# Optimization experiments

Hardware: AMD Instinct MI355X
Metric: run time of the kernel (lower is better)

Reference implementation:

```python
import jax, jax.numpy as jnp
import numpy as np

H, W = 200, 200          # detector resolution
DELX, DELY = 2.0, 2.0    # detector pixel size
EPS = 1e-8


def _rotation(theta, phi, gamma):
    # R = Rz(theta) @ Ry(phi) @ Rx(gamma), as in diffdrr's Rxyz
    ct, st = jnp.cos(theta), jnp.sin(theta)
    cp, sp = jnp.cos(phi), jnp.sin(phi)
    cg, sg = jnp.cos(gamma), jnp.sin(gamma)
    one, zero = jnp.ones_like(ct), jnp.zeros_like(ct)
    Rz = jnp.stack([jnp.stack([ct, -st, zero]), jnp.stack([st, ct, zero]), jnp.stack([zero, zero, one])])
    Ry = jnp.stack([jnp.stack([cp, zero, sp]), jnp.stack([zero, one, zero]), jnp.stack([-sp, zero, cp])])
    Rx = jnp.stack([jnp.stack([one, zero, zero]), jnp.stack([zero, cg, -sg]), jnp.stack([zero, sg, cg])])
    return Rz @ Ry @ Rx


def setup_inputs() -> dict:
    key = jax.random.key(0)
    volume = jax.random.uniform(key, (256, 256, 256), dtype=jnp.float32)
    spacing = jnp.ones((3,), dtype=jnp.float32)
    return {
        "volume": volume,
        "spacing": spacing,
        "sdr": jnp.float32(300.0),
        "theta": jnp.float32(np.pi),
        "phi": jnp.float32(0.0),
        "gamma": jnp.float32(np.pi / 2),
        "bx": jnp.float32(128.0),
        "by": jnp.float32(128.0),
        "bz": jnp.float32(128.0),
    }


def _drr_forward(volume, spacing, sdr, theta, phi, gamma, bx, by, bz):
    # DRR.__init__ flips the volume along axis 0
    vol = volume[::-1]
    nxyz = np.array(vol.shape)  # static shapes: (X, Y, Z)

    # ---- Detector.make_xrays: camera basis, source and detector plane ----
    R = sdr * _rotation(theta, phi, gamma)          # (3,3)
    source = R[:, 0]                                # rho * first column
    center = -source
    u, v = R[:, 1] / sdr, R[:, 2] / sdr             # unit in-plane basis
    t = (jnp.arange(-(H // 2), H // 2) + 1).astype(jnp.float32) * DELX
    s = (jnp.arange(-(W // 2), W // 2) + 1).astype(jnp.float32) * DELY
    trans = jnp.stack([bx, by, bz])
    src = source + trans                            # (3,)
    # cartesian_prod(t, s): row-major (t slow, s fast) -> (H*W, 3)
    tgt = (t[:, None, None] * u + s[None, :, None] * v + center + trans).reshape(H * W, 3)

    # ---- Siddon.raytrace ----
    sdd = tgt - src + EPS                           # (n, 3)
    # alpha values at every axis-aligned voxel boundary plane
    ax = (jnp.arange(nxyz[0] + 1, dtype=jnp.float32) * spacing[0] - src[0]) / sdd[:, 0:1]
    ay = (jnp.arange(nxyz[1] + 1, dtype=jnp.float32) * spacing[1] - src[1]) / sdd[:, 1:2]
    az = (jnp.arange(nxyz[2] + 1, dtype=jnp.float32) * spacing[2] - src[2]) / sdd[:, 2:3]
    alphas = jnp.concatenate([ax, ay, az], axis=-1)  # (n, P) with P = X+Y+Z+3

    # entry/exit alphas of the volume bounding box
    a0 = (0.0 - src) / sdd                           # (n, 3)
    a1 = (nxyz.astype(np.float32) * spacing - src) / sdd
    amin = jnp.max(jnp.minimum(a0, a1), axis=-1, keepdims=True)
    amax = jnp.min(jnp.maximum(a0, a1), axis=-1, keepdims=True)

    good = (alphas >= amin) & (alphas <= amax)
    alphas = jnp.sort(jnp.where(good, alphas, jnp.inf), axis=-1)  # invalid -> +inf at end

    amid = 0.5 * (alphas[:, :-1] + alphas[:, 1:])    # (n, P-1)
    step = alphas[:, 1:] - alphas[:, :-1]            # inf-inf -> nan for padding
    valid = jnp.isfinite(step)

    # midpoint positions -> voxel indices (trunc, as in torch .trunc())
    pts = src + amid[..., None] * sdd[:, None, :]    # (n, P-1, 3)
    idx = jnp.trunc(jnp.where(valid[..., None], pts, 0.0) / spacing).astype(jnp.int32)
    idx = jnp.clip(idx, 0, jnp.asarray(nxyz - 1, dtype=jnp.int32))
    vox = vol[idx[..., 0], idx[..., 1], idx[..., 2]]  # (n, P-1) gather

    drr = jnp.sum(jnp.where(valid, step, 0.0) * vox, axis=-1)  # nansum equivalent
    drr = drr * jnp.linalg.norm(tgt - src + EPS, axis=-1)       # scale by ray length
    return drr.reshape(1, 1, H, W)


def reference(volume, spacing, sdr, theta, phi, gamma, bx, by, bz):
    return _drr_forward(volume, spacing, sdr, theta, phi, gamma, bx, by, bz)
```

## Files before the change

### kernel.cpp

```cpp
#include <hip/hip_runtime.h>
#include <math.h>

#pragma clang fp contract(off)

#define SPLIT 13
#define BATCH 8
static constexpr int HH = 200, WW = 200;
static constexpr int NRAY = HH * WW;
static constexpr int RBLK = 157;
static constexpr int NWG  = RBLK * SPLIT;

__device__ __forceinline__ float alpha_of(float k, float sp, float src, float sdd) {
    return (k * sp - src) / sdd;
}

__device__ __forceinline__ int seed_ptr(float X, float spv, float sr, float sd, bool pos) {
    const float kf = (X * sd + sr) / spv;
    int kk;
    if (pos) {
        kk = (int)floorf(kf) + 1;
        kk = kk < 0 ? 0 : (kk > 257 ? 257 : kk);
        while (kk > 0    && alpha_of((float)(kk-1), spv, sr, sd) >  X) --kk;
        while (kk <= 256 && alpha_of((float)kk,     spv, sr, sd) <= X) ++kk;
    } else {
        kk = (int)ceilf(kf) - 1;
        kk = kk > 256 ? 256 : (kk < -1 ? -1 : kk);
        while (kk < 256 && alpha_of((float)(kk+1), spv, sr, sd) >  X) ++kk;
        while (kk >= 0  && alpha_of((float)kk,     spv, sr, sd) <= X) --kk;
    }
    return kk;
}

#define GEN_INTERVAL(stepv, offv)                                        \
    {   const float q = fminf(fminf(tM0, tM1), tM2);                     \
        stepv = q - prev;                                                \
        const float amid = 0.5f * (prev + q);                            \
        const float p0 = src0 + amid * sdd0;                             \
        const float p1 = src1 + amid * sdd1;                             \
        const float p2 = src2 + amid * sdd2;                             \
        float f0, f1, f2;                                                \
        if (UNIT) { f0 = p0; f1 = p1; f2 = p2; }                         \
        else      { f0 = p0 / spn0; f1 = p1 / spn1; f2 = p2 / spn2; }    \
        f0 = fminf(fmaxf(f0, 0.0f), 255.0f);                             \
        f1 = fminf(fmaxf(f1, 0.0f), 255.0f);                             \
        f2 = fminf(fmaxf(f2, 0.0f), 255.0f);                             \
        const int i0 = (int)f0, i1 = (int)f1, i2 = (int)f2;              \
        offv = (unsigned)(((((255 ^ i0) << 8) + i1) << 8) + i2) << 2;    \
        prev = q;                                                        \
        const bool m0 = (tM0 == q);                                      \
        const bool m1 = !m0 && (tM1 == q);                               \
        const bool m2 = !(m0 || m1);                                     \
        tM0 = m0 ? tM0 + dl0 : tM0;                                      \
        tM1 = m1 ? tM1 + dl1 : tM1;                                      \
        tM2 = m2 ? tM2 + dl2 : tM2; }

template<bool UNIT>
__device__ __forceinline__ float merge_loop(
    const float* __restrict__ vol, int trip, float prev,
    float tM0, float tM1, float tM2,
    float dl0, float dl1, float dl2,
    float src0, float src1, float src2,
    float spn0, float spn1, float spn2,
    float sdd0, float sdd1, float sdd2)
{
    float acc = 0.0f;
    int n = trip;
    while (n >= BATCH) {
        float stepv[BATCH], vox[BATCH];
        unsigned off[BATCH];
        #pragma unroll
        for (int i = 0; i < BATCH; ++i) {
            GEN_INTERVAL(stepv[i], off[i])
            asm volatile("global_load_dword %0, %1, %2"
                         : "=v"(vox[i])
                         : "v"(off[i]), "s"(vol));
        }
        asm volatile("s_waitcnt vmcnt(0)");
        __builtin_amdgcn_sched_barrier(0);
        #pragma unroll
        for (int i = 0; i < BATCH; ++i)
            acc = fmaf(stepv[i], vox[i], acc);
        n -= BATCH;
    }
    while (n > 0) {
        float stepv;
        unsigned off;
        GEN_INTERVAL(stepv, off)
        const float vox = vol[off >> 2];
        acc = fmaf(stepv, vox, acc);
        --n;
    }
    return acc;
}

__global__ __launch_bounds__(256)
void drr_kernel(const float* __restrict__ vol,
                const float* __restrict__ spacing,
                const float* __restrict__ sdrP,
                const float* __restrict__ thetaP,
                const float* __restrict__ phiP,
                const float* __restrict__ gammaP,
                const float* __restrict__ bxP,
                const float* __restrict__ byP,
                const float* __restrict__ bzP,
                float* __restrict__ out)
{
    const int lin = blockIdx.x;
    const int xcd = lin & 7;
    const int pos = lin >> 3;
    const int swz = (xcd == 0) ? pos : (256 + (xcd - 1) * 255 + pos);
    const int ridBlk = swz / SPLIT;
    const int seg    = swz - ridBlk * SPLIT;

    const int rid = ridBlk * 256 + threadIdx.x;
    if (rid >= NRAY) return;
    const int it  = rid % HH;
    const int is  = rid / HH;

    const float sdr = sdrP[0];
    const float th = thetaP[0], ph = phiP[0], ga = gammaP[0];
    const float ct = cosf(th), st = sinf(th);
    const float cp = cosf(ph), sp = sinf(ph);
    const float cg = cosf(ga), sg = sinf(ga);

    const float rot[3][3] = {
        { ct*cp, ct*sp*sg - st*cg, ct*sp*cg + st*sg },
        { st*cp, st*sp*sg + ct*cg, st*sp*cg - ct*sg },
        { -sp,   cp*sg,            cp*cg            }
    };

    float u[3], v[3], source[3], trans[3], src[3], spn[3];
    trans[0] = bxP[0]; trans[1] = byP[0]; trans[2] = bzP[0];
    for (int a = 0; a < 3; ++a) {
        source[a] = sdr * rot[a][0];
        u[a] = (sdr * rot[a][1]) / sdr;
        v[a] = (sdr * rot[a][2]) / sdr;
        src[a] = source[a] + trans[a];
        spn[a] = spacing[a];
    }

    const float tc = (float)(it - HH/2 + 1) * 2.0f;
    const float sc = (float)(is - WW/2 + 1) * 2.0f;

    float sdd[3];
    float nrm2 = 0.0f;
    for (int a = 0; a < 3; ++a) {
        float tg = tc * u[a] + sc * v[a];
        tg = tg - source[a];
        tg = tg + trans[a];
        float dd = (tg - src[a]) + 1e-8f;
        sdd[a] = dd;
        nrm2 = nrm2 + dd * dd;
    }
    const bool unit = (spn[0] == 1.0f) & (spn[1] == 1.0f) & (spn[2] == 1.0f);

    float amin = -INFINITY, amax = INFINITY;
    for (int a = 0; a < 3; ++a) {
        float a0 = (0.0f - src[a]) / sdd[a];
        float a1 = (256.0f * spn[a] - src[a]) / sdd[a];
        amin = fmaxf(amin, fminf(a0, a1));
        amax = fminf(amax, fmaxf(a0, a1));
    }

    float acc = 0.0f;
    if (amax > amin) {
        const float blo = (seg == 0) ? amin
                        : amin + (amax - amin) * ((float)seg / (float)SPLIT);
        const float bhi = (seg == SPLIT - 1) ? amax
                        : amin + (amax - amin) * ((float)(seg + 1) / (float)SPLIT);

        float tM[3], dl[3];
        float prev = -INFINITY;
        int trip = 0;

        for (int a = 0; a < 3; ++a) {
            const float sd = sdd[a], sr = src[a], spv = spn[a];
            const bool pos2 = sd > 0.0f;
            const int ks = seed_ptr(blo, spv, sr, sd, pos2);
            const int ke = seed_ptr(bhi, spv, sr, sd, pos2);
            int cnt;
            if (pos2) {
                cnt = ke - ks;
                if (ks - 1 >= 0) {
                    const float ap = alpha_of((float)(ks-1), spv, sr, sd);
                    if (ap >= amin && ap > prev) prev = ap;
                }
                tM[a] = (ks <= 256) ? alpha_of((float)ks, spv, sr, sd) : INFINITY;
            } else {
                cnt = ks - ke;
                if (ks + 1 <= 256) {
                    const float ap = alpha_of((float)(ks+1), spv, sr, sd);
                    if (ap >= amin && ap > prev) prev = ap;
                }
                tM[a] = (ks >= 0) ? alpha_of((float)ks, spv, sr, sd) : INFINITY;
            }
            if (cnt < 0) cnt = 0;
            trip += cnt;
            dl[a] = fabsf(spv / sd);
        }

        if (unit) {
            acc = merge_loop<true >(vol, trip, prev,
                                    tM[0], tM[1], tM[2], dl[0], dl[1], dl[2],
                                    src[0], src[1], src[2],
                                    spn[0], spn[1], spn[2],
                                    sdd[0], sdd[1], sdd[2]);
        } else {
            acc = merge_loop<false>(vol, trip, prev,
                                    tM[0], tM[1], tM[2], dl[0], dl[1], dl[2],
                                    src[0], src[1], src[2],
                                    spn[0], spn[1], spn[2],
                                    sdd[0], sdd[1], sdd[2]);
        }
    }

    atomicAdd(&out[it * WW + is], acc * sqrtf(nrm2));
}

extern "C" void kernel_launch(void* const* d_in, const int* in_sizes, int n_in,
                              void* d_out, int out_size, void* d_ws, size_t ws_size,
                              hipStream_t stream)
{
    const float* vol     = (const float*)d_in[0];
    const float* spacing = (const float*)d_in[1];
    const float* sdr     = (const float*)d_in[2];
    const float* theta   = (const float*)d_in[3];
    const float* phi     = (const float*)d_in[4];
    const float* gamma   = (const float*)d_in[5];
    const float* bx      = (const float*)d_in[6];
    const float* by      = (const float*)d_in[7];
    const float* bz      = (const float*)d_in[8];
    float* out = (float*)d_out;

    hipMemsetAsync(out, 0, (size_t)out_size * sizeof(float), stream);

    drr_kernel<<<NWG, 256, 0, stream>>>(vol, spacing, sdr, theta, phi, gamma,
                                        bx, by, bz, out);
}
```

Before: 55.15 us.

## Split DRR into precompute, main trace, and deterministic reduction kernels

```diff
diff --git a/kernel.cpp b/kernel.cpp
--- a/kernel.cpp
+++ b/kernel.cpp
@@ -9,6 +9,16 @@
 static constexpr int NRAY = HH * WW;
 static constexpr int RBLK = 157;
 static constexpr int NWG  = RBLK * SPLIT;
+
+static constexpr int WS_SDD0 = 0;
+static constexpr int WS_SDD1 = NRAY;
+static constexpr int WS_SDD2 = 2 * NRAY;
+static constexpr int WS_AMIN = 3 * NRAY;
+static constexpr int WS_AMAX = 4 * NRAY;
+static constexpr int WS_NORM = 5 * NRAY;
+static constexpr int WS_UNI  = 6 * NRAY;
+static constexpr int WS_PART = 6 * NRAY + 8;
+static constexpr size_t WS_BYTES = (size_t)(WS_PART + SPLIT * NRAY) * 4;
 
 __device__ __forceinline__ float alpha_of(float k, float sp, float src, float sdd) {
     return (k * sp - src) / sdd;
@@ -94,16 +104,75 @@
 }
 
 __global__ __launch_bounds__(256)
-void drr_kernel(const float* __restrict__ vol,
-                const float* __restrict__ spacing,
-                const float* __restrict__ sdrP,
-                const float* __restrict__ thetaP,
-                const float* __restrict__ phiP,
-                const float* __restrict__ gammaP,
-                const float* __restrict__ bxP,
-                const float* __restrict__ byP,
-                const float* __restrict__ bzP,
-                float* __restrict__ out)
+void drr_pre(const float* __restrict__ spacing,
+             const float* __restrict__ sdrP,  const float* __restrict__ thetaP,
+             const float* __restrict__ phiP,  const float* __restrict__ gammaP,
+             const float* __restrict__ bxP,   const float* __restrict__ byP,
+             const float* __restrict__ bzP,   float* __restrict__ ws)
+{
+    const int rid = blockIdx.x * blockDim.x + threadIdx.x;
+    if (rid >= NRAY) return;
+    const int it = rid % HH, is = rid / HH;
+
+    const float sdr = sdrP[0];
+    const float th = thetaP[0], ph = phiP[0], ga = gammaP[0];
+    const float ct = cosf(th), st = sinf(th);
+    const float cp = cosf(ph), sp = sinf(ph);
+    const float cg = cosf(ga), sg = sinf(ga);
+
+    const float rot[3][3] = {
+        { ct*cp, ct*sp*sg - st*cg, ct*sp*cg + st*sg },
+        { st*cp, st*sp*sg + ct*cg, st*sp*cg - ct*sg },
+        { -sp,   cp*sg,            cp*cg            }
+    };
+
+    float u[3], v[3], source[3], trans[3], src[3], spn[3];
+    trans[0] = bxP[0]; trans[1] = byP[0]; trans[2] = bzP[0];
+    for (int a = 0; a < 3; ++a) {
+        source[a] = sdr * rot[a][0];
+        u[a] = (sdr * rot[a][1]) / sdr;
+        v[a] = (sdr * rot[a][2]) / sdr;
+        src[a] = source[a] + trans[a];
+        spn[a] = spacing[a];
+    }
+
+    const float tc = (float)(it - HH/2 + 1) * 2.0f;
+    const float sc = (float)(is - WW/2 + 1) * 2.0f;
+
+    float sdd[3];
+    float nrm2 = 0.0f;
+    for (int a = 0; a < 3; ++a) {
+        float tg = tc * u[a] + sc * v[a];
+        tg = tg - source[a];
+        tg = tg + trans[a];
+        float dd = (tg - src[a]) + 1e-8f;
+        sdd[a] = dd;
+        nrm2 = nrm2 + dd * dd;
+    }
+
+    float amin = -INFINITY, amax = INFINITY;
+    for (int a = 0; a < 3; ++a) {
+        float a0 = (0.0f - src[a]) / sdd[a];
+        float a1 = (256.0f * spn[a] - src[a]) / sdd[a];
+        amin = fmaxf(amin, fminf(a0, a1));
+        amax = fminf(amax, fmaxf(a0, a1));
+    }
+
+    ws[WS_SDD0 + rid] = sdd[0];
+    ws[WS_SDD1 + rid] = sdd[1];
+    ws[WS_SDD2 + rid] = sdd[2];
+    ws[WS_AMIN + rid] = amin;
+    ws[WS_AMAX + rid] = amax;
+    ws[WS_NORM + rid] = sqrtf(nrm2);
+    if (rid == 0) {
+        ws[WS_UNI + 0] = src[0]; ws[WS_UNI + 1] = src[1]; ws[WS_UNI + 2] = src[2];
+        ws[WS_UNI + 3] = spn[0]; ws[WS_UNI + 4] = spn[1]; ws[WS_UNI + 5] = spn[2];
+    }
+}
+
+__global__ __launch_bounds__(256)
+void drr_main(const float* __restrict__ vol,
+              float* __restrict__ ws)
 {
     const int lin = blockIdx.x;
     const int xcd = lin & 7;
@@ -114,21 +183,111 @@
 
     const int rid = ridBlk * 256 + threadIdx.x;
     if (rid >= NRAY) return;
-    const int it  = rid % HH;
-    const int is  = rid / HH;
+
+    const float sdd0 = ws[WS_SDD0 + rid];
+    const float sdd1 = ws[WS_SDD1 + rid];
+    const float sdd2 = ws[WS_SDD2 + rid];
+    const float amin = ws[WS_AMIN + rid];
+    const float amax = ws[WS_AMAX + rid];
+    const float src0 = ws[WS_UNI + 0], src1 = ws[WS_UNI + 1], src2 = ws[WS_UNI + 2];
+    const float spn0 = ws[WS_UNI + 3], spn1 = ws[WS_UNI + 4], spn2 = ws[WS_UNI + 5];
+    const bool unit = (spn0 == 1.0f) & (spn1 == 1.0f) & (spn2 == 1.0f);
+
+    float acc = 0.0f;
+    if (amax > amin) {
+        const float blo = (seg == 0) ? amin
+                        : amin + (amax - amin) * ((float)seg / (float)SPLIT);
+        const float bhi = (seg == SPLIT - 1) ? amax
+                        : amin + (amax - amin) * ((float)(seg + 1) / (float)SPLIT);
+
+        const float sddv[3] = { sdd0, sdd1, sdd2 };
+        const float srcv[3] = { src0, src1, src2 };
+        const float spnv[3] = { spn0, spn1, spn2 };
+        float tM[3], dl[3];
+        float prev = -INFINITY;
+        int trip = 0;
+
+        for (int a = 0; a < 3; ++a) {
+            const float sd = sddv[a], sr = srcv[a], spv = spnv[a];
+            const bool pos2 = sd > 0.0f;
+            const int ks = seed_ptr(blo, spv, sr, sd, pos2);
+            const int ke = seed_ptr(bhi, spv, sr, sd, pos2);
+            int cnt;
+            if (pos2) {
+                cnt = ke - ks;
+                if (ks - 1 >= 0) {
+                    const float ap = alpha_of((float)(ks-1), spv, sr, sd);
+                    if (ap >= amin && ap > prev) prev = ap;
+                }
+                tM[a] = (ks <= 256) ? alpha_of((float)ks, spv, sr, sd) : INFINITY;
+            } else {
+                cnt = ks - ke;
+                if (ks + 1 <= 256) {
+                    const float ap = alpha_of((float)(ks+1), spv, sr, sd);
+                    if (ap >= amin && ap > prev) prev = ap;
+                }
+                tM[a] = (ks >= 0) ? alpha_of((float)ks, spv, sr, sd) : INFINITY;
+            }
+            if (cnt < 0) cnt = 0;
+            trip += cnt;
+            dl[a] = fabsf(spv / sd);
+        }
+
+        if (unit) {
+            acc = merge_loop<true >(vol, trip, prev, tM[0], tM[1], tM[2],
+                                    dl[0], dl[1], dl[2], src0, src1, src2,
+                                    spn0, spn1, spn2, sdd0, sdd1, sdd2);
+        } else {
+            acc = merge_loop<false>(vol, trip, prev, tM[0], tM[1], tM[2],
+                                    dl[0], dl[1], dl[2], src0, src1, src2,
+                                    spn0, spn1, spn2, sdd0, sdd1, sdd2);
+        }
+    }
+
+    ws[WS_PART + seg * NRAY + rid] = acc;
+}
+
+__global__ __launch_bounds__(256)
+void drr_fin(const float* __restrict__ ws, float* __restrict__ out)
+{
+    const int rid = blockIdx.x * blockDim.x + threadIdx.x;
+    if (rid >= NRAY) return;
+    float s = 0.0f;
+    #pragma unroll
+    for (int seg = 0; seg < SPLIT; ++seg)
+        s = s + ws[WS_PART + seg * NRAY + rid];
+    const int it = rid % HH, is = rid / HH;
+    out[it * WW + is] = s * ws[WS_NORM + rid];
+}
+
+__global__ __launch_bounds__(256)
+void drr_mono(const float* __restrict__ vol,
+              const float* __restrict__ spacing,
+              const float* __restrict__ sdrP,  const float* __restrict__ thetaP,
+              const float* __restrict__ phiP,  const float* __restrict__ gammaP,
+              const float* __restrict__ bxP,   const float* __restrict__ byP,
+              const float* __restrict__ bzP,   float* __restrict__ out)
+{
+    const int lin = blockIdx.x;
+    const int xcd = lin & 7;
+    const int pos = lin >> 3;
+    const int swz = (xcd == 0) ? pos : (256 + (xcd - 1) * 255 + pos);
+    const int ridBlk = swz / SPLIT;
+    const int seg    = swz - ridBlk * SPLIT;
+    const int rid = ridBlk * 256 + threadIdx.x;
+    if (rid >= NRAY) return;
+    const int it = rid % HH, is = rid / HH;
 
     const float sdr = sdrP[0];
     const float th = thetaP[0], ph = phiP[0], ga = gammaP[0];
     const float ct = cosf(th), st = sinf(th);
     const float cp = cosf(ph), sp = sinf(ph);
     const float cg = cosf(ga), sg = sinf(ga);
-
     const float rot[3][3] = {
         { ct*cp, ct*sp*sg - st*cg, ct*sp*cg + st*sg },
         { st*cp, st*sp*sg + ct*cg, st*sp*cg - ct*sg },
         { -sp,   cp*sg,            cp*cg            }
     };
-
     float u[3], v[3], source[3], trans[3], src[3], spn[3];
     trans[0] = bxP[0]; trans[1] = byP[0]; trans[2] = bzP[0];
     for (int a = 0; a < 3; ++a) {
@@ -138,12 +297,9 @@
         src[a] = source[a] + trans[a];
         spn[a] = spacing[a];
     }
-
     const float tc = (float)(it - HH/2 + 1) * 2.0f;
     const float sc = (float)(is - WW/2 + 1) * 2.0f;
-
-    float sdd[3];
-    float nrm2 = 0.0f;
+    float sdd[3]; float nrm2 = 0.0f;
     for (int a = 0; a < 3; ++a) {
         float tg = tc * u[a] + sc * v[a];
         tg = tg - source[a];
@@ -153,7 +309,6 @@
         nrm2 = nrm2 + dd * dd;
     }
     const bool unit = (spn[0] == 1.0f) & (spn[1] == 1.0f) & (spn[2] == 1.0f);
-
     float amin = -INFINITY, amax = INFINITY;
     for (int a = 0; a < 3; ++a) {
         float a0 = (0.0f - src[a]) / sdd[a];
@@ -161,18 +316,15 @@
         amin = fmaxf(amin, fminf(a0, a1));
         amax = fminf(amax, fmaxf(a0, a1));
     }
-
     float acc = 0.0f;
     if (amax > amin) {
         const float blo = (seg == 0) ? amin
                         : amin + (amax - amin) * ((float)seg / (float)SPLIT);
         const float bhi = (seg == SPLIT - 1) ? amax
                         : amin + (amax - amin) * ((float)(seg + 1) / (float)SPLIT);
-
         float tM[3], dl[3];
         float prev = -INFINITY;
         int trip = 0;
-
         for (int a = 0; a < 3; ++a) {
             const float sd = sdd[a], sr = src[a], spv = spn[a];
             const bool pos2 = sd > 0.0f;
@@ -198,22 +350,16 @@
             trip += cnt;
             dl[a] = fabsf(spv / sd);
         }
-
         if (unit) {
-            acc = merge_loop<true >(vol, trip, prev,
-                                    tM[0], tM[1], tM[2], dl[0], dl[1], dl[2],
-                                    src[0], src[1], src[2],
-                                    spn[0], spn[1], spn[2],
-                                    sdd[0], sdd[1], sdd[2]);
+            acc = merge_loop<true >(vol, trip, prev, tM[0], tM[1], tM[2],
+                                    dl[0], dl[1], dl[2], src[0], src[1], src[2],
+                                    spn[0], spn[1], spn[2], sdd[0], sdd[1], sdd[2]);
         } else {
-            acc = merge_loop<false>(vol, trip, prev,
-                                    tM[0], tM[1], tM[2], dl[0], dl[1], dl[2],
-                                    src[0], src[1], src[2],
-                                    spn[0], spn[1], spn[2],
-                                    sdd[0], sdd[1], sdd[2]);
-        }
-    }
-
+            acc = merge_loop<false>(vol, trip, prev, tM[0], tM[1], tM[2],
+                                    dl[0], dl[1], dl[2], src[0], src[1], src[2],
+                                    spn[0], spn[1], spn[2], sdd[0], sdd[1], sdd[2]);
+        }
+    }
     atomicAdd(&out[it * WW + is], acc * sqrtf(nrm2));
 }
 
@@ -232,8 +378,15 @@
     const float* bz      = (const float*)d_in[8];
     float* out = (float*)d_out;
 
-    hipMemsetAsync(out, 0, (size_t)out_size * sizeof(float), stream);
-
-    drr_kernel<<<NWG, 256, 0, stream>>>(vol, spacing, sdr, theta, phi, gamma,
-                                        bx, by, bz, out);
-}
+    if (ws_size >= WS_BYTES) {
+        float* ws = (float*)d_ws;
+        drr_pre<<<RBLK, 256, 0, stream>>>(spacing, sdr, theta, phi, gamma,
+                                          bx, by, bz, ws);
+        drr_main<<<NWG, 256, 0, stream>>>(vol, ws);
+        drr_fin<<<RBLK, 256, 0, stream>>>(ws, out);
+    } else {
+        hipMemsetAsync(out, 0, (size_t)out_size * sizeof(float), stream);
+        drr_mono<<<NWG, 256, 0, stream>>>(vol, spacing, sdr, theta, phi, gamma,
+                                          bx, by, bz, out);
+    }
+}
```

Result: faster. 52.62 us (-4.6%).
